# Kernel optimization log

Hardware: AMD Instinct MI355X
Metric: run time of the kernel (lower is better)

## Reference

```python
import jax, jax.numpy as jnp
import numpy as np

MAX_DELAY = 128
INPUT = 64
HIDDEN = 128
HALF = HIDDEN // 2
OUT = 64
B = 32
T = 128
OUT_LEN = 64


def setup_inputs() -> dict:
    key = jax.random.key(0)
    ks = jax.random.split(key, 10)
    w = lambda k, sh: (jax.random.normal(k, sh, jnp.float32) * 0.05)
    return {
        "x": jax.random.normal(ks[0], (B, T, INPUT), jnp.float32),
        "lengths": jax.random.randint(ks[1], (B,), 0, T, jnp.int32),
        "out_lengths": OUT_LEN,
        "Wm": w(ks[2], (INPUT + HIDDEN, HIDDEN)), "bm": jnp.zeros((HIDDEN,), jnp.float32),
        "W1": w(ks[3], (HIDDEN, HALF)), "b1": jnp.zeros((HALF,), jnp.float32),
        "W2": w(ks[4], (HALF, 2 * HIDDEN)), "b2": jnp.zeros((2 * HIDDEN,), jnp.float32),
        "Wo": w(ks[5], (HIDDEN, OUT)), "bo": jnp.zeros((OUT,), jnp.float32),
    }


def reference(x, lengths, out_lengths, Wm, bm, W1, b1, W2, b2, Wo, bo):
    # index_tensor: (1, 1, max_delay) in [0, 1)
    index = (jnp.arange(MAX_DELAY, dtype=x.dtype) / MAX_DELAY)[None, None, :]

    def tau_gen(msg):  # msg: (B, H)
        h = jax.nn.relu(msg @ W1 + b1)
        tg = jax.nn.sigmoid(h @ W2 + b2)  # (B, 2H)
        return tg[:, :HIDDEN], tg[:, HIDDEN:]

    def update_buffer(buffer, msg, tau, mem_i):
        # shift left, zero-pad at the end
        new_buf = jnp.pad(buffer[:, :, 1:], ((0, 0), (0, 0), (0, 1)))
        iw = mem_i[..., None] * (1.0 - jnp.abs(tau[..., None] - index)) ** 2  # (B,H,D)
        return (1.0 - iw) * new_buf + iw * msg[..., None]

    masks = (jnp.arange(T) < lengths[:, None]).astype(x.dtype)  # (B, T)

    def enc_step(buffer, inp):
        x_t, mask = inp  # (B, I), (B,)
        m = mask[:, None]  # (B, 1)
        msg = m * jnp.tanh(jnp.concatenate([x_t, buffer[:, :, 0]], axis=-1) @ Wm + bm)
        tau, mem_i = tau_gen(msg)
        new_buf = update_buffer(buffer, msg, tau, mem_i)
        buffer = jnp.where(m[..., None] > 0, new_buf, buffer)
        return buffer, None

    buffer0 = jnp.zeros((B, HIDDEN, MAX_DELAY), x.dtype)
    buffer, _ = jax.lax.scan(enc_step, buffer0, (x.transpose(1, 0, 2), masks.T))

    x0 = jnp.zeros((B, INPUT), x.dtype)

    def dec_step(buffer, _):
        msg = jnp.tanh(jnp.concatenate([x0, buffer[:, :, 0]], axis=-1) @ Wm + bm)
        tau, mem_i = tau_gen(msg)
        buffer = update_buffer(buffer, msg, tau, mem_i)
        return buffer, msg @ Wo + bo

    _, outs = jax.lax.scan(dec_step, buffer, None, length=out_lengths)
    return outs.transpose(1, 0, 2)  # (B, out_lengths, OUT)
```

## Files before the change

kernel.cpp:

```cpp
#include <hip/hip_runtime.h>
#include <math.h>

typedef __attribute__((ext_vector_type(2))) float f32x2;
typedef __attribute__((ext_vector_type(4))) float f32x4;

#define MAX_DELAY 128
#define INPUT 64
#define HIDDEN 128
#define HALF 64
#define OUT 64
#define BATCH 32
#define T 128
#define OUT_LEN 64
#define NTHR 512

static __device__ __forceinline__ f32x2 splat2(float v) { f32x2 r; r.x = v; r.y = v; return r; }
static __device__ __forceinline__ f32x4 splat4(float v) { f32x4 r; r.x = v; r.y = v; r.z = v; r.w = v; return r; }

static __device__ __forceinline__ f32x2 pk_fma(f32x2 a, f32x2 b, f32x2 c) {
    f32x2 d;
    asm("v_pk_fma_f32 %0, %1, %2, %3" : "=v"(d) : "v"(a), "v"(b), "v"(c));
    return d;
}
static __device__ __forceinline__ f32x2 pk_fma_n0(f32x2 a, f32x2 b, f32x2 c) {
    f32x2 d;
    asm("v_pk_fma_f32 %0, %1, %2, %3 neg_lo:[1,0,0] neg_hi:[1,0,0]"
        : "=v"(d) : "v"(a), "v"(b), "v"(c));
    return d;
}
static __device__ __forceinline__ f32x2 pk_add(f32x2 a, f32x2 b) {
    f32x2 d;
    asm("v_pk_add_f32 %0, %1, %2" : "=v"(d) : "v"(a), "v"(b));
    return d;
}
static __device__ __forceinline__ f32x2 lo2(f32x4 v) { f32x2 r; r.x = v.x; r.y = v.y; return r; }
static __device__ __forceinline__ f32x2 hi2(f32x4 v) { f32x2 r; r.x = v.z; r.y = v.w; return r; }

template <int N>
static __device__ __forceinline__ float dotN(const f32x4 (&w)[N], const f32x4* v) {
    f32x2 a0 = splat2(0.f), a1 = splat2(0.f), a2 = splat2(0.f), a3 = splat2(0.f);
#pragma unroll
    for (int j = 0; j < N; ++j) {
        const f32x4 wv = w[j], vv = v[j];
        if (j & 1) { a2 = pk_fma(lo2(wv), lo2(vv), a2); a3 = pk_fma(hi2(wv), hi2(vv), a3); }
        else       { a0 = pk_fma(lo2(wv), lo2(vv), a0); a1 = pk_fma(hi2(wv), hi2(vv), a1); }
    }
    const f32x2 s = pk_add(pk_add(a0, a1), pk_add(a2, a3));
    return s.x + s.y;
}

template <int CTRL>
static __device__ __forceinline__ float dpp_movf(float v) {
    return __int_as_float(__builtin_amdgcn_update_dpp(
        0, __float_as_int(v), CTRL, 0xF, 0xF, true));
}
#define DPP_XOR1 0xB1
#define DPP_XOR2 0x4E
#define DPP_ROT1 0x39
#define DPP_MIR8 0x141

#define PAD16(k) ((k) + (((k) >> 4) << 3))
#define PADH(k)  ((k) + (((k) >> 5) << 2))

__global__ __attribute__((amdgpu_waves_per_eu(2, 2))) __launch_bounds__(NTHR)
void delayrnn_kernel(
    const float* __restrict__ x,
    const int*   __restrict__ lengths,
    const float* __restrict__ Wm,
    const float* __restrict__ bm,
    const float* __restrict__ W1,
    const float* __restrict__ b1,
    const float* __restrict__ W2,
    const float* __restrict__ b2,
    const float* __restrict__ Wo,
    const float* __restrict__ bo,
    float* __restrict__ out)
{
    const int b   = blockIdx.x;
    const int tid = threadIdx.x;
    const int len = lengths[b];
    const int total = len + OUT_LEN;

    const int h  = tid >> 2, q  = tid & 3;
    const int qq = q & 1,    qh = q >> 1;
    const int k1 = tid >> 3, r1 = tid & 7;
    const int co = tid >> 3, ro = tid & 7;
    const int c2 = h + 128 * qh;

    f32x4 wmh[8];
#pragma unroll
    for (int j = 0; j < 8; ++j) {
        wmh[j].x = Wm[(64 + q * 32 + 4 * j    ) * HIDDEN + h];
        wmh[j].y = Wm[(64 + q * 32 + 4 * j + 1) * HIDDEN + h];
        wmh[j].z = Wm[(64 + q * 32 + 4 * j + 2) * HIDDEN + h];
        wmh[j].w = Wm[(64 + q * 32 + 4 * j + 3) * HIDDEN + h];
    }
    f32x4 wmx[4];
#pragma unroll
    for (int j = 0; j < 4; ++j) {
        wmx[j].x = Wm[(q * 16 + 4 * j    ) * HIDDEN + h];
        wmx[j].y = Wm[(q * 16 + 4 * j + 1) * HIDDEN + h];
        wmx[j].z = Wm[(q * 16 + 4 * j + 2) * HIDDEN + h];
        wmx[j].w = Wm[(q * 16 + 4 * j + 3) * HIDDEN + h];
    }
    f32x4 w14[4];
#pragma unroll
    for (int j = 0; j < 4; ++j) {
        w14[j].x = W1[(r1 * 16 + 4 * j    ) * HALF + k1];
        w14[j].y = W1[(r1 * 16 + 4 * j + 1) * HALF + k1];
        w14[j].z = W1[(r1 * 16 + 4 * j + 2) * HALF + k1];
        w14[j].w = W1[(r1 * 16 + 4 * j + 3) * HALF + k1];
    }
    f32x4 w24[8];
#pragma unroll
    for (int j = 0; j < 8; ++j) {
        w24[j].x = W2[(qq * 32 + 4 * j    ) * (2 * HIDDEN) + c2];
        w24[j].y = W2[(qq * 32 + 4 * j + 1) * (2 * HIDDEN) + c2];
        w24[j].z = W2[(qq * 32 + 4 * j + 2) * (2 * HIDDEN) + c2];
        w24[j].w = W2[(qq * 32 + 4 * j + 3) * (2 * HIDDEN) + c2];
    }
    f32x4 wo4[4];
#pragma unroll
    for (int m = 0; m < 4; ++m) {
        wo4[m].x = Wo[(ro * 16 + 4 * m    ) * OUT + co];
        wo4[m].y = Wo[(ro * 16 + 4 * m + 1) * OUT + co];
        wo4[m].z = Wo[(ro * 16 + 4 * m + 2) * OUT + co];
        wo4[m].w = Wo[(ro * 16 + 4 * m + 3) * OUT + co];
    }
    const float bm_r = bm[h];
    const float b1_r = b1[k1];
    const float b2_r = b2[c2];
    const float bo_r = bo[co];

    f32x2 buf2[16];
#pragma unroll
    for (int d = 0; d < 16; ++d) { buf2[d].x = 0.f; buf2[d].y = 0.f; }

    __shared__ f32x4 s_x4[T * INPUT / 4];
    __shared__ float s_vh[140];
    __shared__ f32x4 s_msg4[48];
    __shared__ float s_h1[HALF];
    __shared__ f32x4 s_out4[OUT_LEN * OUT / 4];

    {
        const f32x4* xg4 = (const f32x4*)x;
        for (int idx = tid; idx < T * INPUT / 4; idx += NTHR)
            s_x4[idx] = xg4[b * (T * INPUT / 4) + idx];
        if (tid < 35) ((f32x4*)s_vh)[tid] = splat4(0.f);
    }
    __syncthreads();

    float px = 0.f;
    if (0 < len) px = dotN<4>(wmx, s_x4 + q * 4);

    const float ivb = (float)q * 0.25f;
    float msg_p = 0.f, tau_p = 0.f, mem_p = 0.f;

    for (int i = 0; i < total; ++i) {
        const f32x4* v4 = (const f32x4*)(s_vh + q * 36);
        const float pdot = dotN<8>(wmh, v4);

        {
            float tail_in = dpp_movf<DPP_ROT1>(buf2[0].x);
            if (q == 3) tail_in = 0.f;
            const float taup = tau_p - ivb;
            f32x2 t2; t2.x = taup; t2.y = taup - (1.f / MAX_DELAY);
            const f32x2 st2  = splat2(-2.f / MAX_DELAY);
            const f32x2 mem2 = splat2(mem_p);
            const f32x2 m2m  = splat2(-2.f * mem_p);
            const f32x2 msg2 = splat2(msg_p);
#pragma unroll
            for (int d = 0; d < 16; ++d) {
                f32x2 nb;
                nb.x = buf2[d].y;
                nb.y = (d < 15) ? buf2[d + 1].x : tail_in;
                f32x2 a  = __builtin_elementwise_max(t2, -t2);
                f32x2 f1 = pk_fma(a, mem2, m2m);
                f32x2 iw = pk_fma(a, f1, mem2);
                f32x2 u  = pk_fma(iw, msg2, nb);
                buf2[d]  = pk_fma_n0(iw, nb, u);
                t2 = pk_add(t2, st2);
            }
        }

        float p = pdot + px;
        p += dpp_movf<DPP_XOR1>(p);
        p += dpp_movf<DPP_XOR2>(p);
        const float z  = p + bm_r;
        const float e2 = __expf(2.f * z);
        const float msg = 1.f - 2.f * __builtin_amdgcn_rcpf(e2 + 1.f);
        if (q == 0) ((float*)s_msg4)[PAD16(h)] = msg;
        msg_p = msg;
        __syncthreads();

        {
            const f32x4* m4 = (const f32x4*)((const float*)s_msg4 + r1 * 24);
            float p1 = dotN<4>(w14, m4);
            p1 += dpp_movf<DPP_XOR1>(p1);
            p1 += dpp_movf<DPP_XOR2>(p1);
            p1 += dpp_movf<DPP_MIR8>(p1);
            if (r1 == 0) s_h1[k1] = fmaxf(p1 + b1_r, 0.f);
        }

        px = 0.f;
        if (i + 1 < len) px = dotN<4>(wmx, s_x4 + (i + 1) * 16 + q * 4);

        if (i >= len) {
            const f32x4* mo4 = (const f32x4*)((const float*)s_msg4 + ro * 24);
            float po = dotN<4>(wo4, mo4);
            po += dpp_movf<DPP_XOR1>(po);
            po += dpp_movf<DPP_XOR2>(po);
            po += dpp_movf<DPP_MIR8>(po);
            if (ro == 0) ((float*)s_out4)[(i - len) * OUT + co] = po + bo_r;
        }
        __syncthreads();

        {
            const f32x4* hh4 = (const f32x4*)(s_h1 + (qq << 5));
            float pt = dotN<8>(w24, hh4);
            pt += dpp_movf<DPP_XOR1>(pt);
            const float own = __builtin_amdgcn_rcpf(1.f + __expf(-(pt + b2_r)));
            const float oth = dpp_movf<DPP_XOR2>(own);
            const float tau_r = qh ? oth : own;
            const float mem_r = qh ? own : oth;
            tau_p = tau_r; mem_p = mem_r;

            const float nb0 = buf2[0].y;
            const float iw0 = tau_r * (tau_r * mem_r - 2.f * mem_r) + mem_r;
            const float head = iw0 * (msg_p - nb0) + nb0;
            if (q == 0) s_vh[PADH(h)] = head;
        }
        __syncthreads();
    }

    {
        f32x4* og4 = (f32x4*)(out + b * OUT_LEN * OUT);
        og4[tid]        = s_out4[tid];
        og4[tid + NTHR] = s_out4[tid + NTHR];
    }
}

extern "C" void kernel_launch(void* const* d_in, const int* in_sizes, int n_in,
                              void* d_out, int out_size, void* d_ws, size_t ws_size,
                              hipStream_t stream) {
    const float* x       = (const float*)d_in[0];
    const int*   lengths = (const int*)  d_in[1];
    const float* Wm = (const float*)d_in[3];
    const float* bm = (const float*)d_in[4];
    const float* W1 = (const float*)d_in[5];
    const float* b1 = (const float*)d_in[6];
    const float* W2 = (const float*)d_in[7];
    const float* b2 = (const float*)d_in[8];
    const float* Wo = (const float*)d_in[9];
    const float* bo = (const float*)d_in[10];
    float* out = (float*)d_out;

    delayrnn_kernel<<<BATCH, NTHR, 0, stream>>>(
        x, lengths, Wm, bm, W1, b1, W2, b2, Wo, bo, out);
}
```

Baseline: 315.4 us.

## Halve block size to 256 threads with two lanes per hidden unit

Each hidden unit's work is now split across 2 lanes instead of 4, giving 4 waves per block instead of 8. Each thread holds twice as many weights and buffer registers, and cross-lane reductions use fewer DPP steps. The aim is cheaper __syncthreads barriers and fewer reduction steps along the sequential recurrence. In exchange each thread does twice the serial FMA work per step and uses many more VGPRs (waves_per_eu set to 1).

```diff
diff --git a/kernel.cpp b/kernel.cpp
--- a/kernel.cpp
+++ b/kernel.cpp
@@ -12,7 +12,7 @@
 #define BATCH 32
 #define T 128
 #define OUT_LEN 64
-#define NTHR 512
+#define NTHR 256
 
 static __device__ __forceinline__ f32x2 splat2(float v) { f32x2 r; r.x = v; r.y = v; return r; }
 static __device__ __forceinline__ f32x4 splat4(float v) { f32x4 r; r.x = v; r.y = v; r.z = v; r.w = v; return r; }
@@ -56,13 +56,11 @@
 }
 #define DPP_XOR1 0xB1
 #define DPP_XOR2 0x4E
-#define DPP_ROT1 0x39
-#define DPP_MIR8 0x141
-
-#define PAD16(k) ((k) + (((k) >> 4) << 3))
-#define PADH(k)  ((k) + (((k) >> 5) << 2))
-
-__global__ __attribute__((amdgpu_waves_per_eu(2, 2))) __launch_bounds__(NTHR)
+
+#define PAD32(k)  ((k) + (((k) >> 5) << 2))
+#define PADH64(k) ((k) + (((k) >> 6) << 3))
+
+__global__ __attribute__((amdgpu_waves_per_eu(1, 1))) __launch_bounds__(NTHR)
 void delayrnn_kernel(
     const float* __restrict__ x,
     const int*   __restrict__ lengths,
@@ -81,64 +79,63 @@
     const int len = lengths[b];
     const int total = len + OUT_LEN;
 
-    const int h  = tid >> 2, q  = tid & 3;
-    const int qq = q & 1,    qh = q >> 1;
-    const int k1 = tid >> 3, r1 = tid & 7;
-    const int co = tid >> 3, ro = tid & 7;
-    const int c2 = h + 128 * qh;
-
-    f32x4 wmh[8];
+    const int h  = tid >> 1, e  = tid & 1;
+    const int k1 = tid >> 2, r1 = tid & 3;
+    const int co = tid >> 2, ro = tid & 3;
+    const int c2 = h + 128 * e;
+
+    f32x4 wmh[16];
+#pragma unroll
+    for (int j = 0; j < 16; ++j) {
+        wmh[j].x = Wm[(64 + e * 64 + 4 * j    ) * HIDDEN + h];
+        wmh[j].y = Wm[(64 + e * 64 + 4 * j + 1) * HIDDEN + h];
+        wmh[j].z = Wm[(64 + e * 64 + 4 * j + 2) * HIDDEN + h];
+        wmh[j].w = Wm[(64 + e * 64 + 4 * j + 3) * HIDDEN + h];
+    }
+    f32x4 wmx[8];
 #pragma unroll
     for (int j = 0; j < 8; ++j) {
-        wmh[j].x = Wm[(64 + q * 32 + 4 * j    ) * HIDDEN + h];
-        wmh[j].y = Wm[(64 + q * 32 + 4 * j + 1) * HIDDEN + h];
-        wmh[j].z = Wm[(64 + q * 32 + 4 * j + 2) * HIDDEN + h];
-        wmh[j].w = Wm[(64 + q * 32 + 4 * j + 3) * HIDDEN + h];
-    }
-    f32x4 wmx[4];
-#pragma unroll
-    for (int j = 0; j < 4; ++j) {
-        wmx[j].x = Wm[(q * 16 + 4 * j    ) * HIDDEN + h];
-        wmx[j].y = Wm[(q * 16 + 4 * j + 1) * HIDDEN + h];
-        wmx[j].z = Wm[(q * 16 + 4 * j + 2) * HIDDEN + h];
-        wmx[j].w = Wm[(q * 16 + 4 * j + 3) * HIDDEN + h];
-    }
-    f32x4 w14[4];
-#pragma unroll
-    for (int j = 0; j < 4; ++j) {
-        w14[j].x = W1[(r1 * 16 + 4 * j    ) * HALF + k1];
-        w14[j].y = W1[(r1 * 16 + 4 * j + 1) * HALF + k1];
-        w14[j].z = W1[(r1 * 16 + 4 * j + 2) * HALF + k1];
-        w14[j].w = W1[(r1 * 16 + 4 * j + 3) * HALF + k1];
-    }
-    f32x4 w24[8];
+        wmx[j].x = Wm[(e * 32 + 4 * j    ) * HIDDEN + h];
+        wmx[j].y = Wm[(e * 32 + 4 * j + 1) * HIDDEN + h];
+        wmx[j].z = Wm[(e * 32 + 4 * j + 2) * HIDDEN + h];
+        wmx[j].w = Wm[(e * 32 + 4 * j + 3) * HIDDEN + h];
+    }
+    f32x4 w14[8];
 #pragma unroll
     for (int j = 0; j < 8; ++j) {
-        w24[j].x = W2[(qq * 32 + 4 * j    ) * (2 * HIDDEN) + c2];
-        w24[j].y = W2[(qq * 32 + 4 * j + 1) * (2 * HIDDEN) + c2];
-        w24[j].z = W2[(qq * 32 + 4 * j + 2) * (2 * HIDDEN) + c2];
-        w24[j].w = W2[(qq * 32 + 4 * j + 3) * (2 * HIDDEN) + c2];
-    }
-    f32x4 wo4[4];
-#pragma unroll
-    for (int m = 0; m < 4; ++m) {
-        wo4[m].x = Wo[(ro * 16 + 4 * m    ) * OUT + co];
-        wo4[m].y = Wo[(ro * 16 + 4 * m + 1) * OUT + co];
-        wo4[m].z = Wo[(ro * 16 + 4 * m + 2) * OUT + co];
-        wo4[m].w = Wo[(ro * 16 + 4 * m + 3) * OUT + co];
+        w14[j].x = W1[(r1 * 32 + 4 * j    ) * HALF + k1];
+        w14[j].y = W1[(r1 * 32 + 4 * j + 1) * HALF + k1];
+        w14[j].z = W1[(r1 * 32 + 4 * j + 2) * HALF + k1];
+        w14[j].w = W1[(r1 * 32 + 4 * j + 3) * HALF + k1];
+    }
+    f32x4 w24[16];
+#pragma unroll
+    for (int j = 0; j < 16; ++j) {
+        w24[j].x = W2[(4 * j    ) * (2 * HIDDEN) + c2];
+        w24[j].y = W2[(4 * j + 1) * (2 * HIDDEN) + c2];
+        w24[j].z = W2[(4 * j + 2) * (2 * HIDDEN) + c2];
+        w24[j].w = W2[(4 * j + 3) * (2 * HIDDEN) + c2];
+    }
+    f32x4 wo4[8];
+#pragma unroll
+    for (int m = 0; m < 8; ++m) {
+        wo4[m].x = Wo[(ro * 32 + 4 * m    ) * OUT + co];
+        wo4[m].y = Wo[(ro * 32 + 4 * m + 1) * OUT + co];
+        wo4[m].z = Wo[(ro * 32 + 4 * m + 2) * OUT + co];
+        wo4[m].w = Wo[(ro * 32 + 4 * m + 3) * OUT + co];
     }
     const float bm_r = bm[h];
     const float b1_r = b1[k1];
     const float b2_r = b2[c2];
     const float bo_r = bo[co];
 
-    f32x2 buf2[16];
-#pragma unroll
-    for (int d = 0; d < 16; ++d) { buf2[d].x = 0.f; buf2[d].y = 0.f; }
+    f32x2 buf2[32];
+#pragma unroll
+    for (int d = 0; d < 32; ++d) { buf2[d].x = 0.f; buf2[d].y = 0.f; }
 
     __shared__ f32x4 s_x4[T * INPUT / 4];
-    __shared__ float s_vh[140];
-    __shared__ f32x4 s_msg4[48];
+    __shared__ float s_vh[136];
+    __shared__ float s_msg[144];
     __shared__ float s_h1[HALF];
     __shared__ f32x4 s_out4[OUT_LEN * OUT / 4];
 
@@ -146,23 +143,23 @@
         const f32x4* xg4 = (const f32x4*)x;
         for (int idx = tid; idx < T * INPUT / 4; idx += NTHR)
             s_x4[idx] = xg4[b * (T * INPUT / 4) + idx];
-        if (tid < 35) ((f32x4*)s_vh)[tid] = splat4(0.f);
+        if (tid < 34) ((f32x4*)s_vh)[tid] = splat4(0.f);
     }
     __syncthreads();
 
     float px = 0.f;
-    if (0 < len) px = dotN<4>(wmx, s_x4 + q * 4);
-
-    const float ivb = (float)q * 0.25f;
+    if (0 < len) px = dotN<8>(wmx, s_x4 + e * 8);
+
+    const float ivb = (float)e * 0.5f;
     float msg_p = 0.f, tau_p = 0.f, mem_p = 0.f;
 
     for (int i = 0; i < total; ++i) {
-        const f32x4* v4 = (const f32x4*)(s_vh + q * 36);
-        const float pdot = dotN<8>(wmh, v4);
+        const f32x4* v4 = (const f32x4*)(s_vh + e * 72);
+        const float pdot = dotN<16>(wmh, v4);
 
         {
-            float tail_in = dpp_movf<DPP_ROT1>(buf2[0].x);
-            if (q == 3) tail_in = 0.f;
+            float tail_in = dpp_movf<DPP_XOR1>(buf2[0].x);
+            if (e == 1) tail_in = 0.f;
             const float taup = tau_p - ivb;
             f32x2 t2; t2.x = taup; t2.y = taup - (1.f / MAX_DELAY);
             const f32x2 st2  = splat2(-2.f / MAX_DELAY);
@@ -170,10 +167,10 @@
             const f32x2 m2m  = splat2(-2.f * mem_p);
             const f32x2 msg2 = splat2(msg_p);
 #pragma unroll
-            for (int d = 0; d < 16; ++d) {
+            for (int d = 0; d < 32; ++d) {
                 f32x2 nb;
                 nb.x = buf2[d].y;
-                nb.y = (d < 15) ? buf2[d + 1].x : tail_in;
+                nb.y = (d < 31) ? buf2[d + 1].x : tail_in;
                 f32x2 a  = __builtin_elementwise_max(t2, -t2);
                 f32x2 f1 = pk_fma(a, mem2, m2m);
                 f32x2 iw = pk_fma(a, f1, mem2);
@@ -185,58 +182,56 @@
 
         float p = pdot + px;
         p += dpp_movf<DPP_XOR1>(p);
-        p += dpp_movf<DPP_XOR2>(p);
         const float z  = p + bm_r;
         const float e2 = __expf(2.f * z);
         const float msg = 1.f - 2.f * __builtin_amdgcn_rcpf(e2 + 1.f);
-        if (q == 0) ((float*)s_msg4)[PAD16(h)] = msg;
+        if (e == 0) s_msg[PAD32(h)] = msg;
         msg_p = msg;
         __syncthreads();
 
         {
-            const f32x4* m4 = (const f32x4*)((const float*)s_msg4 + r1 * 24);
-            float p1 = dotN<4>(w14, m4);
+            const f32x4* m4 = (const f32x4*)(s_msg + r1 * 36);
+            float p1 = dotN<8>(w14, m4);
             p1 += dpp_movf<DPP_XOR1>(p1);
             p1 += dpp_movf<DPP_XOR2>(p1);
-            p1 += dpp_movf<DPP_MIR8>(p1);
             if (r1 == 0) s_h1[k1] = fmaxf(p1 + b1_r, 0.f);
         }
 
         px = 0.f;
-        if (i + 1 < len) px = dotN<4>(wmx, s_x4 + (i + 1) * 16 + q * 4);
+        if (i + 1 < len) px = dotN<8>(wmx, s_x4 + (i + 1) * 16 + e * 8);
 
         if (i >= len) {
-            const f32x4* mo4 = (const f32x4*)((const float*)s_msg4 + ro * 24);
-            float po = dotN<4>(wo4, mo4);
+            const f32x4* mo4 = (const f32x4*)(s_msg + ro * 36);
+            float po = dotN<8>(wo4, mo4);
             po += dpp_movf<DPP_XOR1>(po);
             po += dpp_movf<DPP_XOR2>(po);
-            po += dpp_movf<DPP_MIR8>(po);
             if (ro == 0) ((float*)s_out4)[(i - len) * OUT + co] = po + bo_r;
         }
         __syncthreads();
 
         {
-            const f32x4* hh4 = (const f32x4*)(s_h1 + (qq << 5));
-            float pt = dotN<8>(w24, hh4);
-            pt += dpp_movf<DPP_XOR1>(pt);
+            const f32x4* hh4 = (const f32x4*)s_h1;
+            const float pt = dotN<16>(w24, hh4);
             const float own = __builtin_amdgcn_rcpf(1.f + __expf(-(pt + b2_r)));
-            const float oth = dpp_movf<DPP_XOR2>(own);
-            const float tau_r = qh ? oth : own;
-            const float mem_r = qh ? own : oth;
+            const float oth = dpp_movf<DPP_XOR1>(own);
+            const float tau_r = e ? oth : own;
+            const float mem_r = e ? own : oth;
             tau_p = tau_r; mem_p = mem_r;
 
             const float nb0 = buf2[0].y;
             const float iw0 = tau_r * (tau_r * mem_r - 2.f * mem_r) + mem_r;
             const float head = iw0 * (msg_p - nb0) + nb0;
-            if (q == 0) s_vh[PADH(h)] = head;
+            if (e == 0) s_vh[PADH64(h)] = head;
         }
         __syncthreads();
     }
 
     {
         f32x4* og4 = (f32x4*)(out + b * OUT_LEN * OUT);
-        og4[tid]        = s_out4[tid];
-        og4[tid + NTHR] = s_out4[tid + NTHR];
+        og4[tid]            = s_out4[tid];
+        og4[tid + NTHR]     = s_out4[tid + NTHR];
+        og4[tid + 2 * NTHR] = s_out4[tid + 2 * NTHR];
+        og4[tid + 3 * NTHR] = s_out4[tid + 3 * NTHR];
     }
 }
 
```

After: 484.9 us. +53.8%, slower.

## Compute W1 layer with wave-local partial sums and LDS atomics to drop a barrier

Applied to the files above, without the earlier changes.

Each wave now computes a partial W1 projection from the 16 message values that it wrote itself, then adds the partial into a double-buffered shared accumulator preset with the bias. This removes one __syncthreads per recurrent step, leaving two instead of three. ReLU moves to the point where the W2 stage reads the accumulator. The output projection and the next-x prefetch move after the tau/mem stage. In exchange it adds LDS atomic contention across eight waves and relies on wave-local ordering of LDS writes and reads.

```diff
diff --git a/kernel.cpp b/kernel.cpp
--- a/kernel.cpp
+++ b/kernel.cpp
@@ -83,7 +83,7 @@
 
     const int h  = tid >> 2, q  = tid & 3;
     const int qq = q & 1,    qh = q >> 1;
-    const int k1 = tid >> 3, r1 = tid & 7;
+    const int wv = tid >> 6, ln = tid & 63;
     const int co = tid >> 3, ro = tid & 7;
     const int c2 = h + 128 * qh;
 
@@ -103,13 +103,11 @@
         wmx[j].z = Wm[(q * 16 + 4 * j + 2) * HIDDEN + h];
         wmx[j].w = Wm[(q * 16 + 4 * j + 3) * HIDDEN + h];
     }
-    f32x4 w14[4];
-#pragma unroll
-    for (int j = 0; j < 4; ++j) {
-        w14[j].x = W1[(r1 * 16 + 4 * j    ) * HALF + k1];
-        w14[j].y = W1[(r1 * 16 + 4 * j + 1) * HALF + k1];
-        w14[j].z = W1[(r1 * 16 + 4 * j + 2) * HALF + k1];
-        w14[j].w = W1[(r1 * 16 + 4 * j + 3) * HALF + k1];
+    f32x2 w1s[8];
+#pragma unroll
+    for (int j = 0; j < 8; ++j) {
+        w1s[j].x = W1[(16 * wv + 2 * j    ) * HALF + ln];
+        w1s[j].y = W1[(16 * wv + 2 * j + 1) * HALF + ln];
     }
     f32x4 w24[8];
 #pragma unroll
@@ -128,7 +126,7 @@
         wo4[m].w = Wo[(ro * 16 + 4 * m + 3) * OUT + co];
     }
     const float bm_r = bm[h];
-    const float b1_r = b1[k1];
+    const float b1z = b1[ln];
     const float b2_r = b2[c2];
     const float bo_r = bo[co];
 
@@ -138,8 +136,8 @@
 
     __shared__ f32x4 s_x4[T * INPUT / 4];
     __shared__ float s_vh[140];
-    __shared__ f32x4 s_msg4[48];
-    __shared__ float s_h1[HALF];
+    __shared__ float s_msg[192];
+    __shared__ float s_h1acc[2][HALF];
     __shared__ f32x4 s_out4[OUT_LEN * OUT / 4];
 
     {
@@ -147,6 +145,7 @@
         for (int idx = tid; idx < T * INPUT / 4; idx += NTHR)
             s_x4[idx] = xg4[b * (T * INPUT / 4) + idx];
         if (tid < 35) ((f32x4*)s_vh)[tid] = splat4(0.f);
+        if (tid < 64) s_h1acc[0][tid] = b1z;
     }
     __syncthreads();
 
@@ -157,6 +156,10 @@
     float msg_p = 0.f, tau_p = 0.f, mem_p = 0.f;
 
     for (int i = 0; i < total; ++i) {
+        const int par = i & 1;
+
+        if (tid < 64) s_h1acc[par ^ 1][ln] = b1z;
+
         const f32x4* v4 = (const f32x4*)(s_vh + q * 36);
         const float pdot = dotN<8>(wmh, v4);
 
@@ -189,35 +192,37 @@
         const float z  = p + bm_r;
         const float e2 = __expf(2.f * z);
         const float msg = 1.f - 2.f * __builtin_amdgcn_rcpf(e2 + 1.f);
-        if (q == 0) ((float*)s_msg4)[PAD16(h)] = msg;
+        if (q == 0) s_msg[PAD16(h)] = msg;
         msg_p = msg;
+
+        {
+            const f32x2* m2 = (const f32x2*)(s_msg + 24 * wv);
+            f32x2 acc0 = pk_fma(w1s[0], m2[0], splat2(0.f));
+            f32x2 acc1 = pk_fma(w1s[1], m2[1], splat2(0.f));
+            acc0 = pk_fma(w1s[2], m2[2], acc0);
+            acc1 = pk_fma(w1s[3], m2[3], acc1);
+            acc0 = pk_fma(w1s[4], m2[4], acc0);
+            acc1 = pk_fma(w1s[5], m2[5], acc1);
+            acc0 = pk_fma(w1s[6], m2[6], acc0);
+            acc1 = pk_fma(w1s[7], m2[7], acc1);
+            const f32x2 s = pk_add(acc0, acc1);
+            atomicAdd(&s_h1acc[par][ln], s.x + s.y);
+        }
         __syncthreads();
 
         {
-            const f32x4* m4 = (const f32x4*)((const float*)s_msg4 + r1 * 24);
-            float p1 = dotN<4>(w14, m4);
-            p1 += dpp_movf<DPP_XOR1>(p1);
-            p1 += dpp_movf<DPP_XOR2>(p1);
-            p1 += dpp_movf<DPP_MIR8>(p1);
-            if (r1 == 0) s_h1[k1] = fmaxf(p1 + b1_r, 0.f);
-        }
-
-        px = 0.f;
-        if (i + 1 < len) px = dotN<4>(wmx, s_x4 + (i + 1) * 16 + q * 4);
-
-        if (i >= len) {
-            const f32x4* mo4 = (const f32x4*)((const float*)s_msg4 + ro * 24);
-            float po = dotN<4>(wo4, mo4);
-            po += dpp_movf<DPP_XOR1>(po);
-            po += dpp_movf<DPP_XOR2>(po);
-            po += dpp_movf<DPP_MIR8>(po);
-            if (ro == 0) ((float*)s_out4)[(i - len) * OUT + co] = po + bo_r;
-        }
-        __syncthreads();
-
-        {
-            const f32x4* hh4 = (const f32x4*)(s_h1 + (qq << 5));
-            float pt = dotN<8>(w24, hh4);
+            const f32x4* hh4 = (const f32x4*)(s_h1acc[par] + (qq << 5));
+            const f32x4 z4 = splat4(0.f);
+            f32x2 a0 = splat2(0.f), a1 = splat2(0.f), a2 = splat2(0.f), a3 = splat2(0.f);
+#pragma unroll
+            for (int j = 0; j < 8; ++j) {
+                const f32x4 hr = __builtin_elementwise_max(hh4[j], z4);
+                const f32x4 wvv = w24[j];
+                if (j & 1) { a2 = pk_fma(lo2(wvv), lo2(hr), a2); a3 = pk_fma(hi2(wvv), hi2(hr), a3); }
+                else       { a0 = pk_fma(lo2(wvv), lo2(hr), a0); a1 = pk_fma(hi2(wvv), hi2(hr), a1); }
+            }
+            const f32x2 ssum = pk_add(pk_add(a0, a1), pk_add(a2, a3));
+            float pt = ssum.x + ssum.y;
             pt += dpp_movf<DPP_XOR1>(pt);
             const float own = __builtin_amdgcn_rcpf(1.f + __expf(-(pt + b2_r)));
             const float oth = dpp_movf<DPP_XOR2>(own);
@@ -230,6 +235,19 @@
             const float head = iw0 * (msg_p - nb0) + nb0;
             if (q == 0) s_vh[PADH(h)] = head;
         }
+
+        if (i >= len) {
+            const f32x4* mo4 = (const f32x4*)(s_msg + ro * 24);
+            float po = dotN<4>(wo4, mo4);
+            po += dpp_movf<DPP_XOR1>(po);
+            po += dpp_movf<DPP_XOR2>(po);
+            po += dpp_movf<DPP_MIR8>(po);
+            if (ro == 0) ((float*)s_out4)[(i - len) * OUT + co] = po + bo_r;
+        }
+
+        px = 0.f;
+        if (i + 1 < len) px = dotN<4>(wmx, s_x4 + (i + 1) * 16 + q * 4);
+
         __syncthreads();
     }
 
```

New measurement: 436.6 us. 1.38x slower.
